# Kernel tuning notes

Hardware: AMD Instinct MI355X
Metric: run time of the kernel (lower is better)

## Reference

```python
import jax, jax.numpy as jnp
import numpy as np

B, S, F, H = 256, 1024, 64, 64

def setup_inputs() -> dict:
    key = jax.random.key(0)
    ks = jax.random.split(key, 6)
    x = jax.random.normal(ks[0], (B, S, F), dtype=jnp.float32)
    # Keras LSTM params: kernel [F,4H], recurrent_kernel [H,4H], bias [4H] (gate order i,f,c,o)
    kernel = jax.random.normal(ks[1], (F, 4 * H), dtype=jnp.float32) * (1.0 / np.sqrt(F))
    rec_kernel = jax.random.normal(ks[2], (H, 4 * H), dtype=jnp.float32) * (1.0 / np.sqrt(H))
    bias = jnp.zeros((4 * H,), dtype=jnp.float32)
    dense_w = jax.random.normal(ks[3], (H, 1), dtype=jnp.float32) * (1.0 / np.sqrt(H))
    dense_b = jnp.zeros((1,), dtype=jnp.float32)
    return {"x": x, "kernel": kernel, "rec_kernel": rec_kernel, "bias": bias,
            "dense_w": dense_w, "dense_b": dense_b}

def reference(x, kernel, rec_kernel, bias, dense_w, dense_b):
    # Precompute input contribution for all timesteps: [B,S,4H]
    xz = jnp.einsum('bsf,fg->bsg', x, kernel) + bias
    xz_t = jnp.transpose(xz, (1, 0, 2))  # [S,B,4H]

    def step(carry, xz_step):
        h, c = carry
        z = xz_step + h @ rec_kernel  # [B,4H]
        zi, zf, zc, zo = jnp.split(z, 4, axis=-1)
        i = jax.nn.sigmoid(zi)
        f = jax.nn.sigmoid(zf)
        o = jax.nn.sigmoid(zo)
        c_new = f * c + i * jnp.tanh(zc)
        h_new = o * jnp.tanh(c_new)
        return (h_new, c_new), h_new

    h0 = jnp.zeros((x.shape[0], rec_kernel.shape[0]), dtype=x.dtype)
    c0 = jnp.zeros_like(h0)
    _, hs = jax.lax.scan(step, (h0, c0), xz_t)  # hs: [S,B,H]
    hs = jnp.transpose(hs, (1, 0, 2))  # [B,S,H]
    out = jax.nn.sigmoid(hs @ dense_w + dense_b)  # [B,S,1]
    return out
```

## Files before the change

kernel.cpp:

```cpp
#include <hip/hip_runtime.h>

typedef __attribute__((ext_vector_type(8))) short short8;
typedef __attribute__((ext_vector_type(4))) float f32x4;

#define SS 1024
#define NBLK 64
#define HROW 72

__device__ __forceinline__ float sigmoidf_(float x) {
    return __builtin_amdgcn_rcpf(1.0f + __expf(-x));
}
__device__ __forceinline__ float tanhf_(float x) {
    return 1.0f - 2.0f * __builtin_amdgcn_rcpf(__expf(2.0f * x) + 1.0f);
}
__device__ __forceinline__ unsigned short f2bf(float f) {
    unsigned int u = __float_as_uint(f);
    u += 0x7fffu + ((u >> 16) & 1u);
    return (unsigned short)(u >> 16);
}
__device__ __forceinline__ float bf2f(unsigned short u) {
    return __uint_as_float((unsigned int)u << 16);
}
__device__ __forceinline__ float h2f_lo(unsigned int u) {
    _Float16 h; unsigned short s = (unsigned short)(u & 0xffffu);
    __builtin_memcpy(&h, &s, 2); return (float)h;
}
__device__ __forceinline__ float h2f_hi(unsigned int u) {
    _Float16 h; unsigned short s = (unsigned short)(u >> 16);
    __builtin_memcpy(&h, &s, 2); return (float)h;
}
__device__ __forceinline__ unsigned int pkf16(float a, float b) {
    auto p = __builtin_amdgcn_cvt_pkrtz(a, b);
    unsigned int u; __builtin_memcpy(&u, &p, 4); return u;
}

#define RAW_BARRIER() asm volatile("s_waitcnt lgkmcnt(0)\n\ts_barrier" ::: "memory")

#define MF(A, Bv, C) __builtin_amdgcn_mfma_f32_16x16x32_bf16(A, Bv, C, 0, 0, 0)

__global__ __launch_bounds__(256)
void xzgemm(const float* __restrict__ x, const float* __restrict__ wk,
            const float* __restrict__ bias, uint2* __restrict__ xzp) {
    const int tid = threadIdx.x;
    const int l   = tid & 63;
    const int w   = tid >> 6;
    const int m   = l & 15;
    const int q   = l >> 4;

    short8 Bf[16][2];
    float  bv[16];
#pragma unroll
    for (int ct = 0; ct < 16; ++ct) {
        bv[ct] = bias[ct * 16 + m];
#pragma unroll
        for (int h2 = 0; h2 < 2; ++h2) {
            short8 v;
#pragma unroll
            for (int j = 0; j < 8; ++j)
                v[j] = (short)f2bf(wk[(h2 * 32 + q * 8 + j) * 256 + ct * 16 + m]);
            Bf[ct][h2] = v;
        }
    }

    const int wt = blockIdx.x * 4 + w;
    for (int it = 0; it < 16; ++it) {
        const int ti = wt * 16 + it;
        const float* __restrict__ xr = x + (size_t)(ti * 16 + m) * 64;
        const float4 a0 = *(const float4*)(xr + q * 8);
        const float4 a1 = *(const float4*)(xr + q * 8 + 4);
        const float4 b0 = *(const float4*)(xr + 32 + q * 8);
        const float4 b1 = *(const float4*)(xr + 32 + q * 8 + 4);
        short8 xa0, xa1;
        xa0[0] = (short)f2bf(a0.x); xa0[1] = (short)f2bf(a0.y);
        xa0[2] = (short)f2bf(a0.z); xa0[3] = (short)f2bf(a0.w);
        xa0[4] = (short)f2bf(a1.x); xa0[5] = (short)f2bf(a1.y);
        xa0[6] = (short)f2bf(a1.z); xa0[7] = (short)f2bf(a1.w);
        xa1[0] = (short)f2bf(b0.x); xa1[1] = (short)f2bf(b0.y);
        xa1[2] = (short)f2bf(b0.z); xa1[3] = (short)f2bf(b0.w);
        xa1[4] = (short)f2bf(b1.x); xa1[5] = (short)f2bf(b1.y);
        xa1[6] = (short)f2bf(b1.z); xa1[7] = (short)f2bf(b1.w);

#pragma unroll
        for (int ctn = 0; ctn < 4; ++ctn) {
            const f32x4 ci = {bv[ctn],      bv[ctn],      bv[ctn],      bv[ctn]};
            const f32x4 cf = {bv[ctn + 4],  bv[ctn + 4],  bv[ctn + 4],  bv[ctn + 4]};
            const f32x4 cc = {bv[ctn + 8],  bv[ctn + 8],  bv[ctn + 8],  bv[ctn + 8]};
            const f32x4 co = {bv[ctn + 12], bv[ctn + 12], bv[ctn + 12], bv[ctn + 12]};
            const f32x4 zi = MF(xa1, Bf[ctn][1],      MF(xa0, Bf[ctn][0],      ci));
            const f32x4 zf = MF(xa1, Bf[ctn + 4][1],  MF(xa0, Bf[ctn + 4][0],  cf));
            const f32x4 zc = MF(xa1, Bf[ctn + 8][1],  MF(xa0, Bf[ctn + 8][0],  cc));
            const f32x4 zo = MF(xa1, Bf[ctn + 12][1], MF(xa0, Bf[ctn + 12][0], co));
            uint2* __restrict__ ob =
                xzp + ((size_t)(ti * 16 + q * 4) * 64 + ctn * 16 + m);
#pragma unroll
            for (int r = 0; r < 4; ++r) {
                uint2 v;
                v.x = pkf16(zi[r], zf[r]);
                v.y = pkf16(zc[r], zo[r]);
                ob[(size_t)r * 64] = v;
            }
        }
    }
}

#define LOADB(VAR, G, KC) do {                                                \
    const int kb = ((KC) << 5) + (q << 3);                                    \
    const int nn = ((G) << 6) + n0;                                           \
    short8 v;                                                                 \
    v[0] = (short)f2bf(rk[(kb + 0) * 256 + nn]);                              \
    v[1] = (short)f2bf(rk[(kb + 1) * 256 + nn]);                              \
    v[2] = (short)f2bf(rk[(kb + 2) * 256 + nn]);                              \
    v[3] = (short)f2bf(rk[(kb + 3) * 256 + nn]);                              \
    v[4] = (short)f2bf(rk[(kb + 4) * 256 + nn]);                              \
    v[5] = (short)f2bf(rk[(kb + 5) * 256 + nn]);                              \
    v[6] = (short)f2bf(rk[(kb + 6) * 256 + nn]);                              \
    v[7] = (short)f2bf(rk[(kb + 7) * 256 + nn]);                              \
    VAR = v; } while (0)

#define REGION(T, PAR, P, DO_O) do {                                           \
    const short8 ha0 = *(const short8*)&hbuf[(PAR) ^ 1][m * HROW + (q << 3)];  \
    const short8 ha1 = *(const short8*)&hbuf[(PAR) ^ 1][m * HROW + 32 + (q << 3)]; \
    const uint2 cur = P;                                                       \
    P = xb[(size_t)(((T) + 2 < SS) ? (T) + 2 : SS - 1) << 6];                  \
    const float vi = h2f_lo(cur.x), vf = h2f_hi(cur.x);                        \
    const float vc = h2f_lo(cur.y), vo = h2f_hi(cur.y);                        \
    const f32x4 cgi = {vi, vi, vi, vi};                                        \
    const f32x4 cgf = {vf, vf, vf, vf};                                        \
    const f32x4 cgc = {vc, vc, vc, vc};                                        \
    const f32x4 cgo = {vo, vo, vo, vo};                                        \
    const f32x4 zc = MF(ha1, BHC1, MF(ha0, BHC0, cgc));                        \
    const f32x4 zo = MF(ha1, BHO1, MF(ha0, BHO0, cgo));                        \
    const f32x4 zi = MF(ha1, BHI1, MF(ha0, BHI0, cgi));                        \
    const f32x4 zf = MF(ha1, BHF1, MF(ha0, BHF0, cgf));                        \
    if (DM == 1 && (DO_O) && w == 0) {                                         \
        const f32x4 zz = {0.f, 0.f, 0.f, 0.f};                                 \
        const f32x4 z4 = MF(ha1, BD1, MF(ha0, BD0, zz));                       \
        if (m == 0) {                                                          \
            out[((size_t)((bb << 2) + q) << 10) + (T) - 1] =                   \
                sigmoidf_(z4[0] + db0);                                        \
        }                                                                      \
    }                                                                          \
    const float tc = tanhf_(zc[0]);                                            \
    const float go = sigmoidf_(zo[0]);                                         \
    const float gi = sigmoidf_(zi[0]);                                         \
    const float gf = sigmoidf_(zf[0]);                                         \
    cc0 = gf * cc0 + gi * tc;                                                  \
    const float h0 = go * tanhf_(cc0);                                         \
    const unsigned short hb16 = f2bf(h0);                                      \
    hbuf[PAR][(q << 2) * HROW + n0] = (short)hb16;                             \
    if (DM == 0) hb[(size_t)(T) << 6] = hb16;                                  \
    RAW_BARRIER();                                                             \
} while (0)

template<int DM>
__global__ __launch_bounds__(256, 1)
void lstm_xz(const uint2* __restrict__ xzu, const float* __restrict__ rk,
             unsigned short* __restrict__ hg, const float* __restrict__ dw,
             const float* __restrict__ db, float* __restrict__ out) {
    const int bb  = blockIdx.x;
    const int tid = threadIdx.x;
    const int l   = tid & 63;
    const int w   = tid >> 6;
    const int m   = l & 15;
    const int q   = l >> 4;
    const int n0  = (w << 4) + m;

    __shared__ short hbuf[2][16 * HROW];

    for (int i = tid; i < 2 * 16 * HROW; i += 256) ((short*)hbuf)[i] = 0;
    __syncthreads();

    short8 BHI0, BHI1, BHF0, BHF1, BHC0, BHC1, BHO0, BHO1;
    LOADB(BHI0, 0, 0); LOADB(BHI1, 0, 1);
    LOADB(BHF0, 1, 0); LOADB(BHF1, 1, 1);
    LOADB(BHC0, 2, 0); LOADB(BHC1, 2, 1);
    LOADB(BHO0, 3, 0); LOADB(BHO1, 3, 1);

    short8 BD0, BD1;
    {
        short8 v0 = {0, 0, 0, 0, 0, 0, 0, 0}, v1 = v0;
        if (m == 0) {
#pragma unroll
            for (int i = 0; i < 8; ++i) v0[i] = (short)f2bf(dw[(q << 3) + i]);
#pragma unroll
            for (int i = 0; i < 8; ++i) v1[i] = (short)f2bf(dw[32 + (q << 3) + i]);
        }
        BD0 = v0; BD1 = v1;
    }
    const float db0 = db[0];

    const size_t base = ((size_t)((bb << 2) + q) << 16) + n0;
    const uint2* __restrict__ xb = xzu + base;
    unsigned short* __restrict__ hb = hg + base;

    uint2 PA = xb[0], PB = xb[64];
    float cc0 = 0.f;

    REGION(0, 0, PA, 0);
    REGION(1, 1, PB, 1);
    for (int t = 2; t < SS; t += 2) {
        REGION(t,     0, PA, 1);
        REGION(t + 1, 1, PB, 1);
    }
    if (DM == 1 && w == 0) {
        const short8 ha0 = *(const short8*)&hbuf[1][m * HROW + (q << 3)];
        const short8 ha1 = *(const short8*)&hbuf[1][m * HROW + 32 + (q << 3)];
        const f32x4 zz = {0.f, 0.f, 0.f, 0.f};
        const f32x4 z4 = MF(ha1, BD1, MF(ha0, BD0, zz));
        if (m == 0) {
            out[((size_t)((bb << 2) + q) << 10) + SS - 1] =
                sigmoidf_(z4[0] + db0);
        }
    }
}

__global__ __launch_bounds__(256)
void dense_out(const unsigned short* __restrict__ hg,
               const float* __restrict__ dw, const float* __restrict__ db,
               float* __restrict__ out) {
    const int row = blockIdx.x * 256 + threadIdx.x;
    const short8* __restrict__ hr = (const short8*)(hg + (size_t)row * 64);
    float acc = db[0];
#pragma unroll
    for (int jj = 0; jj < 8; ++jj) {
        const short8 v = hr[jj];
#pragma unroll
        for (int k = 0; k < 8; ++k)
            acc += bf2f((unsigned short)v[k]) * dw[jj * 8 + k];
    }
    out[row] = sigmoidf_(acc);
}

extern "C" void kernel_launch(void* const* d_in, const int* in_sizes, int n_in,
                              void* d_out, int out_size, void* d_ws, size_t ws_size,
                              hipStream_t stream) {
    const float* x    = (const float*)d_in[0];
    const float* wk   = (const float*)d_in[1];
    const float* rk   = (const float*)d_in[2];
    const float* bias = (const float*)d_in[3];
    const float* dw   = (const float*)d_in[4];
    const float* db   = (const float*)d_in[5];
    float* out = (float*)d_out;

    const size_t XZ_BYTES = (size_t)262144 * 256 * 2;
    const size_t HG_BYTES = (size_t)262144 * 64 * 2;

    uint2* xz = (uint2*)d_ws;
    hipLaunchKernelGGL(xzgemm, dim3(256), dim3(256), 0, stream,
                       x, wk, bias, xz);

    if (ws_size >= XZ_BYTES + HG_BYTES) {
        unsigned short* hg = (unsigned short*)((char*)d_ws + XZ_BYTES);
        hipLaunchKernelGGL((lstm_xz<0>), dim3(NBLK), dim3(256), 0, stream,
                           xz, rk, hg, dw, db, out);
        hipLaunchKernelGGL(dense_out, dim3(1024), dim3(256), 0, stream,
                           hg, dw, db, out);
    } else {
        hipLaunchKernelGGL((lstm_xz<1>), dim3(NBLK), dim3(256), 0, stream,
                           xz, rk, (unsigned short*)nullptr, dw, db, out);
    }
}
```

Baseline: 426.7 us.

## Interleave two independent batch groups per LSTM block, halving block count

```diff
diff --git a/kernel.cpp b/kernel.cpp
--- a/kernel.cpp
+++ b/kernel.cpp
@@ -4,7 +4,7 @@
 typedef __attribute__((ext_vector_type(4))) float f32x4;
 
 #define SS 1024
-#define NBLK 64
+#define NBLK 32
 #define HROW 72
 
 __device__ __forceinline__ float sigmoidf_(float x) {
@@ -63,8 +63,8 @@
     }
 
     const int wt = blockIdx.x * 4 + w;
-    for (int it = 0; it < 16; ++it) {
-        const int ti = wt * 16 + it;
+    for (int it = 0; it < 4; ++it) {
+        const int ti = wt * 4 + it;
         const float* __restrict__ xr = x + (size_t)(ti * 16 + m) * 64;
         const float4 a0 = *(const float4*)(xr + q * 8);
         const float4 a1 = *(const float4*)(xr + q * 8 + 4);
@@ -117,46 +117,55 @@
     v[7] = (short)f2bf(rk[(kb + 7) * 256 + nn]);                              \
     VAR = v; } while (0)
 
-#define REGION(T, PAR, P, DO_O) do {                                           \
-    const short8 ha0 = *(const short8*)&hbuf[(PAR) ^ 1][m * HROW + (q << 3)];  \
-    const short8 ha1 = *(const short8*)&hbuf[(PAR) ^ 1][m * HROW + 32 + (q << 3)]; \
-    const uint2 cur = P;                                                       \
-    P = xb[(size_t)(((T) + 2 < SS) ? (T) + 2 : SS - 1) << 6];                  \
-    const float vi = h2f_lo(cur.x), vf = h2f_hi(cur.x);                        \
-    const float vc = h2f_lo(cur.y), vo = h2f_hi(cur.y);                        \
-    const f32x4 cgi = {vi, vi, vi, vi};                                        \
-    const f32x4 cgf = {vf, vf, vf, vf};                                        \
-    const f32x4 cgc = {vc, vc, vc, vc};                                        \
-    const f32x4 cgo = {vo, vo, vo, vo};                                        \
-    const f32x4 zc = MF(ha1, BHC1, MF(ha0, BHC0, cgc));                        \
-    const f32x4 zo = MF(ha1, BHO1, MF(ha0, BHO0, cgo));                        \
-    const f32x4 zi = MF(ha1, BHI1, MF(ha0, BHI0, cgi));                        \
-    const f32x4 zf = MF(ha1, BHF1, MF(ha0, BHF0, cgf));                        \
-    if (DM == 1 && (DO_O) && w == 0) {                                         \
-        const f32x4 zz = {0.f, 0.f, 0.f, 0.f};                                 \
-        const f32x4 z4 = MF(ha1, BD1, MF(ha0, BD0, zz));                       \
-        if (m == 0) {                                                          \
-            out[((size_t)((bb << 2) + q) << 10) + (T) - 1] =                   \
-                sigmoidf_(z4[0] + db0);                                        \
-        }                                                                      \
-    }                                                                          \
-    const float tc = tanhf_(zc[0]);                                            \
-    const float go = sigmoidf_(zo[0]);                                         \
-    const float gi = sigmoidf_(zi[0]);                                         \
-    const float gf = sigmoidf_(zf[0]);                                         \
-    cc0 = gf * cc0 + gi * tc;                                                  \
-    const float h0 = go * tanhf_(cc0);                                         \
-    const unsigned short hb16 = f2bf(h0);                                      \
-    hbuf[PAR][(q << 2) * HROW + n0] = (short)hb16;                             \
-    if (DM == 0) hb[(size_t)(T) << 6] = hb16;                                  \
+#define REGION2(T, PAR, Pa, Pb) do {                                           \
+    const short8 a0 = *(const short8*)&hbufA[(PAR) ^ 1][m * HROW + (q << 3)];  \
+    const short8 a1 = *(const short8*)&hbufA[(PAR) ^ 1][m * HROW + 32 + (q << 3)]; \
+    const short8 b0 = *(const short8*)&hbufB[(PAR) ^ 1][m * HROW + (q << 3)];  \
+    const short8 b1 = *(const short8*)&hbufB[(PAR) ^ 1][m * HROW + 32 + (q << 3)]; \
+    const uint2 curA = Pa; const uint2 curB = Pb;                              \
+    { const size_t xo = (size_t)(((T) + 2 < SS) ? (T) + 2 : SS - 1) << 6;      \
+      Pa = xbA[xo]; Pb = xbB[xo]; }                                            \
+    const float viA = h2f_lo(curA.x), vfA = h2f_hi(curA.x);                    \
+    const float vcA = h2f_lo(curA.y), voA = h2f_hi(curA.y);                    \
+    const float viB = h2f_lo(curB.x), vfB = h2f_hi(curB.x);                    \
+    const float vcB = h2f_lo(curB.y), voB = h2f_hi(curB.y);                    \
+    const f32x4 cgcA = {vcA, vcA, vcA, vcA};                                   \
+    const f32x4 cgoA = {voA, voA, voA, voA};                                   \
+    const f32x4 cgiA = {viA, viA, viA, viA};                                   \
+    const f32x4 cgfA = {vfA, vfA, vfA, vfA};                                   \
+    const f32x4 cgcB = {vcB, vcB, vcB, vcB};                                   \
+    const f32x4 cgoB = {voB, voB, voB, voB};                                   \
+    const f32x4 cgiB = {viB, viB, viB, viB};                                   \
+    const f32x4 cgfB = {vfB, vfB, vfB, vfB};                                   \
+    const f32x4 zcA = MF(a1, BHC1, MF(a0, BHC0, cgcA));                        \
+    const f32x4 zcB = MF(b1, BHC1, MF(b0, BHC0, cgcB));                        \
+    const f32x4 zoA = MF(a1, BHO1, MF(a0, BHO0, cgoA));                        \
+    const f32x4 zoB = MF(b1, BHO1, MF(b0, BHO0, cgoB));                        \
+    const f32x4 ziA = MF(a1, BHI1, MF(a0, BHI0, cgiA));                        \
+    const f32x4 ziB = MF(b1, BHI1, MF(b0, BHI0, cgiB));                        \
+    const f32x4 zfA = MF(a1, BHF1, MF(a0, BHF0, cgfA));                        \
+    const f32x4 zfB = MF(b1, BHF1, MF(b0, BHF0, cgfB));                        \
+    const float tcA = tanhf_(zcA[0]);                                          \
+    const float tcB = tanhf_(zcB[0]);                                          \
+    const float goA = sigmoidf_(zoA[0]), giA = sigmoidf_(ziA[0]);              \
+    const float gfA = sigmoidf_(zfA[0]);                                       \
+    const float goB = sigmoidf_(zoB[0]), giB = sigmoidf_(ziB[0]);              \
+    const float gfB = sigmoidf_(zfB[0]);                                       \
+    ccA = gfA * ccA + giA * tcA;                                               \
+    ccB = gfB * ccB + giB * tcB;                                               \
+    const float hA = goA * tanhf_(ccA);                                        \
+    const float hB = goB * tanhf_(ccB);                                        \
+    const unsigned short hA16 = f2bf(hA), hB16 = f2bf(hB);                     \
+    hbufA[PAR][(q << 2) * HROW + n0] = (short)hA16;                            \
+    hbufB[PAR][(q << 2) * HROW + n0] = (short)hB16;                            \
+    hbA[(size_t)(T) << 6] = hA16;                                              \
+    hbB[(size_t)(T) << 6] = hB16;                                              \
     RAW_BARRIER();                                                             \
 } while (0)
 
-template<int DM>
 __global__ __launch_bounds__(256, 1)
-void lstm_xz(const uint2* __restrict__ xzu, const float* __restrict__ rk,
-             unsigned short* __restrict__ hg, const float* __restrict__ dw,
-             const float* __restrict__ db, float* __restrict__ out) {
+void lstm_g2(const uint2* __restrict__ xzu, const float* __restrict__ rk,
+             unsigned short* __restrict__ hg) {
     const int bb  = blockIdx.x;
     const int tid = threadIdx.x;
     const int l   = tid & 63;
@@ -165,9 +174,13 @@
     const int q   = l >> 4;
     const int n0  = (w << 4) + m;
 
-    __shared__ short hbuf[2][16 * HROW];
-
-    for (int i = tid; i < 2 * 16 * HROW; i += 256) ((short*)hbuf)[i] = 0;
+    __shared__ short hbufA[2][16 * HROW];
+    __shared__ short hbufB[2][16 * HROW];
+
+    for (int i = tid; i < 2 * 16 * HROW; i += 256) {
+        ((short*)hbufA)[i] = 0;
+        ((short*)hbufB)[i] = 0;
+    }
     __syncthreads();
 
     short8 BHI0, BHI1, BHF0, BHF1, BHC0, BHC1, BHO0, BHO1;
@@ -176,41 +189,22 @@
     LOADB(BHC0, 2, 0); LOADB(BHC1, 2, 1);
     LOADB(BHO0, 3, 0); LOADB(BHO1, 3, 1);
 
-    short8 BD0, BD1;
-    {
-        short8 v0 = {0, 0, 0, 0, 0, 0, 0, 0}, v1 = v0;
-        if (m == 0) {
-#pragma unroll
-            for (int i = 0; i < 8; ++i) v0[i] = (short)f2bf(dw[(q << 3) + i]);
-#pragma unroll
-            for (int i = 0; i < 8; ++i) v1[i] = (short)f2bf(dw[32 + (q << 3) + i]);
-        }
-        BD0 = v0; BD1 = v1;
-    }
-    const float db0 = db[0];
-
-    const size_t base = ((size_t)((bb << 2) + q) << 16) + n0;
-    const uint2* __restrict__ xb = xzu + base;
-    unsigned short* __restrict__ hb = hg + base;
-
-    uint2 PA = xb[0], PB = xb[64];
-    float cc0 = 0.f;
-
-    REGION(0, 0, PA, 0);
-    REGION(1, 1, PB, 1);
+    const size_t baseA = ((size_t)((bb << 3) + q) << 16) + n0;
+    const size_t baseB = ((size_t)((bb << 3) + 4 + q) << 16) + n0;
+    const uint2* __restrict__ xbA = xzu + baseA;
+    const uint2* __restrict__ xbB = xzu + baseB;
+    unsigned short* __restrict__ hbA = hg + baseA;
+    unsigned short* __restrict__ hbB = hg + baseB;
+
+    uint2 QA = xbA[0], RA = xbA[64];
+    uint2 QB = xbB[0], RB = xbB[64];
+    float ccA = 0.f, ccB = 0.f;
+
+    REGION2(0, 0, QA, QB);
+    REGION2(1, 1, RA, RB);
     for (int t = 2; t < SS; t += 2) {
-        REGION(t,     0, PA, 1);
-        REGION(t + 1, 1, PB, 1);
-    }
-    if (DM == 1 && w == 0) {
-        const short8 ha0 = *(const short8*)&hbuf[1][m * HROW + (q << 3)];
-        const short8 ha1 = *(const short8*)&hbuf[1][m * HROW + 32 + (q << 3)];
-        const f32x4 zz = {0.f, 0.f, 0.f, 0.f};
-        const f32x4 z4 = MF(ha1, BD1, MF(ha0, BD0, zz));
-        if (m == 0) {
-            out[((size_t)((bb << 2) + q) << 10) + SS - 1] =
-                sigmoidf_(z4[0] + db0);
-        }
+        REGION2(t,     0, QA, QB);
+        REGION2(t + 1, 1, RA, RB);
     }
 }
 
@@ -243,20 +237,13 @@
     float* out = (float*)d_out;
 
     const size_t XZ_BYTES = (size_t)262144 * 256 * 2;
-    const size_t HG_BYTES = (size_t)262144 * 64 * 2;
-
     uint2* xz = (uint2*)d_ws;
-    hipLaunchKernelGGL(xzgemm, dim3(256), dim3(256), 0, stream,
+    unsigned short* hg = (unsigned short*)((char*)d_ws + XZ_BYTES);
+
+    hipLaunchKernelGGL(xzgemm, dim3(1024), dim3(256), 0, stream,
                        x, wk, bias, xz);
-
-    if (ws_size >= XZ_BYTES + HG_BYTES) {
-        unsigned short* hg = (unsigned short*)((char*)d_ws + XZ_BYTES);
-        hipLaunchKernelGGL((lstm_xz<0>), dim3(NBLK), dim3(256), 0, stream,
-                           xz, rk, hg, dw, db, out);
-        hipLaunchKernelGGL(dense_out, dim3(1024), dim3(256), 0, stream,
-                           hg, dw, db, out);
-    } else {
-        hipLaunchKernelGGL((lstm_xz<1>), dim3(NBLK), dim3(256), 0, stream,
-                           xz, rk, (unsigned short*)nullptr, dw, db, out);
-    }
-}
+    hipLaunchKernelGGL(lstm_g2, dim3(NBLK), dim3(256), 0, stream,
+                       xz, rk, hg);
+    hipLaunchKernelGGL(dense_out, dim3(1024), dim3(256), 0, stream,
+                       hg, dw, db, out);
+}
```

New measurement: 607.8 us. 42.4% more time.

## Fuse input projection into recurrent kernel via producer warps and LDS ring

Applied to the files above, without the earlier changes.

```diff
diff --git a/kernel.cpp b/kernel.cpp
--- a/kernel.cpp
+++ b/kernel.cpp
@@ -38,108 +38,34 @@
 
 #define MF(A, Bv, C) __builtin_amdgcn_mfma_f32_16x16x32_bf16(A, Bv, C, 0, 0, 0)
 
-__global__ __launch_bounds__(256)
-void xzgemm(const float* __restrict__ x, const float* __restrict__ wk,
-            const float* __restrict__ bias, uint2* __restrict__ xzp) {
-    const int tid = threadIdx.x;
-    const int l   = tid & 63;
-    const int w   = tid >> 6;
-    const int m   = l & 15;
-    const int q   = l >> 4;
-
-    short8 Bf[16][2];
-    float  bv[16];
-#pragma unroll
-    for (int ct = 0; ct < 16; ++ct) {
-        bv[ct] = bias[ct * 16 + m];
-#pragma unroll
-        for (int h2 = 0; h2 < 2; ++h2) {
-            short8 v;
-#pragma unroll
-            for (int j = 0; j < 8; ++j)
-                v[j] = (short)f2bf(wk[(h2 * 32 + q * 8 + j) * 256 + ct * 16 + m]);
-            Bf[ct][h2] = v;
-        }
-    }
-
-    const int wt = blockIdx.x * 4 + w;
-    for (int it = 0; it < 16; ++it) {
-        const int ti = wt * 16 + it;
-        const float* __restrict__ xr = x + (size_t)(ti * 16 + m) * 64;
-        const float4 a0 = *(const float4*)(xr + q * 8);
-        const float4 a1 = *(const float4*)(xr + q * 8 + 4);
-        const float4 b0 = *(const float4*)(xr + 32 + q * 8);
-        const float4 b1 = *(const float4*)(xr + 32 + q * 8 + 4);
-        short8 xa0, xa1;
-        xa0[0] = (short)f2bf(a0.x); xa0[1] = (short)f2bf(a0.y);
-        xa0[2] = (short)f2bf(a0.z); xa0[3] = (short)f2bf(a0.w);
-        xa0[4] = (short)f2bf(a1.x); xa0[5] = (short)f2bf(a1.y);
-        xa0[6] = (short)f2bf(a1.z); xa0[7] = (short)f2bf(a1.w);
-        xa1[0] = (short)f2bf(b0.x); xa1[1] = (short)f2bf(b0.y);
-        xa1[2] = (short)f2bf(b0.z); xa1[3] = (short)f2bf(b0.w);
-        xa1[4] = (short)f2bf(b1.x); xa1[5] = (short)f2bf(b1.y);
-        xa1[6] = (short)f2bf(b1.z); xa1[7] = (short)f2bf(b1.w);
-
-#pragma unroll
-        for (int ctn = 0; ctn < 4; ++ctn) {
-            const f32x4 ci = {bv[ctn],      bv[ctn],      bv[ctn],      bv[ctn]};
-            const f32x4 cf = {bv[ctn + 4],  bv[ctn + 4],  bv[ctn + 4],  bv[ctn + 4]};
-            const f32x4 cc = {bv[ctn + 8],  bv[ctn + 8],  bv[ctn + 8],  bv[ctn + 8]};
-            const f32x4 co = {bv[ctn + 12], bv[ctn + 12], bv[ctn + 12], bv[ctn + 12]};
-            const f32x4 zi = MF(xa1, Bf[ctn][1],      MF(xa0, Bf[ctn][0],      ci));
-            const f32x4 zf = MF(xa1, Bf[ctn + 4][1],  MF(xa0, Bf[ctn + 4][0],  cf));
-            const f32x4 zc = MF(xa1, Bf[ctn + 8][1],  MF(xa0, Bf[ctn + 8][0],  cc));
-            const f32x4 zo = MF(xa1, Bf[ctn + 12][1], MF(xa0, Bf[ctn + 12][0], co));
-            uint2* __restrict__ ob =
-                xzp + ((size_t)(ti * 16 + q * 4) * 64 + ctn * 16 + m);
-#pragma unroll
-            for (int r = 0; r < 4; ++r) {
-                uint2 v;
-                v.x = pkf16(zi[r], zf[r]);
-                v.y = pkf16(zc[r], zo[r]);
-                ob[(size_t)r * 64] = v;
-            }
-        }
-    }
-}
-
-#define LOADB(VAR, G, KC) do {                                                \
+
+#define LOADB(VAR, G, KC, SRC, NN) do {                                       \
     const int kb = ((KC) << 5) + (q << 3);                                    \
-    const int nn = ((G) << 6) + n0;                                           \
     short8 v;                                                                 \
-    v[0] = (short)f2bf(rk[(kb + 0) * 256 + nn]);                              \
-    v[1] = (short)f2bf(rk[(kb + 1) * 256 + nn]);                              \
-    v[2] = (short)f2bf(rk[(kb + 2) * 256 + nn]);                              \
-    v[3] = (short)f2bf(rk[(kb + 3) * 256 + nn]);                              \
-    v[4] = (short)f2bf(rk[(kb + 4) * 256 + nn]);                              \
-    v[5] = (short)f2bf(rk[(kb + 5) * 256 + nn]);                              \
-    v[6] = (short)f2bf(rk[(kb + 6) * 256 + nn]);                              \
-    v[7] = (short)f2bf(rk[(kb + 7) * 256 + nn]);                              \
+    v[0] = (short)f2bf(SRC[(kb + 0) * 256 + (NN)]);                           \
+    v[1] = (short)f2bf(SRC[(kb + 1) * 256 + (NN)]);                           \
+    v[2] = (short)f2bf(SRC[(kb + 2) * 256 + (NN)]);                           \
+    v[3] = (short)f2bf(SRC[(kb + 3) * 256 + (NN)]);                           \
+    v[4] = (short)f2bf(SRC[(kb + 4) * 256 + (NN)]);                           \
+    v[5] = (short)f2bf(SRC[(kb + 5) * 256 + (NN)]);                           \
+    v[6] = (short)f2bf(SRC[(kb + 6) * 256 + (NN)]);                           \
+    v[7] = (short)f2bf(SRC[(kb + 7) * 256 + (NN)]);                           \
     VAR = v; } while (0)
 
-#define REGION(T, PAR, P, DO_O) do {                                           \
+#define CREGION(T, PAR) do {                                                   \
     const short8 ha0 = *(const short8*)&hbuf[(PAR) ^ 1][m * HROW + (q << 3)];  \
     const short8 ha1 = *(const short8*)&hbuf[(PAR) ^ 1][m * HROW + 32 + (q << 3)]; \
-    const uint2 cur = P;                                                       \
-    P = xb[(size_t)(((T) + 2 < SS) ? (T) + 2 : SS - 1) << 6];                  \
+    const uint2 cur = ring[(T) & 1][q][n0];                                    \
     const float vi = h2f_lo(cur.x), vf = h2f_hi(cur.x);                        \
     const float vc = h2f_lo(cur.y), vo = h2f_hi(cur.y);                        \
+    const f32x4 cgc = {vc, vc, vc, vc};                                        \
+    const f32x4 cgo = {vo, vo, vo, vo};                                        \
     const f32x4 cgi = {vi, vi, vi, vi};                                        \
     const f32x4 cgf = {vf, vf, vf, vf};                                        \
-    const f32x4 cgc = {vc, vc, vc, vc};                                        \
-    const f32x4 cgo = {vo, vo, vo, vo};                                        \
     const f32x4 zc = MF(ha1, BHC1, MF(ha0, BHC0, cgc));                        \
     const f32x4 zo = MF(ha1, BHO1, MF(ha0, BHO0, cgo));                        \
     const f32x4 zi = MF(ha1, BHI1, MF(ha0, BHI0, cgi));                        \
     const f32x4 zf = MF(ha1, BHF1, MF(ha0, BHF0, cgf));                        \
-    if (DM == 1 && (DO_O) && w == 0) {                                         \
-        const f32x4 zz = {0.f, 0.f, 0.f, 0.f};                                 \
-        const f32x4 z4 = MF(ha1, BD1, MF(ha0, BD0, zz));                       \
-        if (m == 0) {                                                          \
-            out[((size_t)((bb << 2) + q) << 10) + (T) - 1] =                   \
-                sigmoidf_(z4[0] + db0);                                        \
-        }                                                                      \
-    }                                                                          \
     const float tc = tanhf_(zc[0]);                                            \
     const float go = sigmoidf_(zo[0]);                                         \
     const float gi = sigmoidf_(zi[0]);                                         \
@@ -148,68 +74,106 @@
     const float h0 = go * tanhf_(cc0);                                         \
     const unsigned short hb16 = f2bf(h0);                                      \
     hbuf[PAR][(q << 2) * HROW + n0] = (short)hb16;                             \
-    if (DM == 0) hb[(size_t)(T) << 6] = hb16;                                  \
+    hb[(size_t)(T) << 6] = hb16;                                               \
     RAW_BARRIER();                                                             \
 } while (0)
 
-template<int DM>
-__global__ __launch_bounds__(256, 1)
-void lstm_xz(const uint2* __restrict__ xzu, const float* __restrict__ rk,
-             unsigned short* __restrict__ hg, const float* __restrict__ dw,
-             const float* __restrict__ db, float* __restrict__ out) {
+#define PPROD(S, RPS, F0, F1, F2, F3) do {                                     \
+    if ((S) < SS) {                                                            \
+        short8 xa0, xa1;                                                       \
+        xa0[0] = (short)f2bf(F0.x); xa0[1] = (short)f2bf(F0.y);                \
+        xa0[2] = (short)f2bf(F0.z); xa0[3] = (short)f2bf(F0.w);                \
+        xa0[4] = (short)f2bf(F1.x); xa0[5] = (short)f2bf(F1.y);                \
+        xa0[6] = (short)f2bf(F1.z); xa0[7] = (short)f2bf(F1.w);                \
+        xa1[0] = (short)f2bf(F2.x); xa1[1] = (short)f2bf(F2.y);                \
+        xa1[2] = (short)f2bf(F2.z); xa1[3] = (short)f2bf(F2.w);                \
+        xa1[4] = (short)f2bf(F3.x); xa1[5] = (short)f2bf(F3.y);                \
+        xa1[6] = (short)f2bf(F3.z); xa1[7] = (short)f2bf(F3.w);                \
+        const f32x4 zi = MF(xa1, WI1, MF(xa0, WI0, cbi));                      \
+        const f32x4 zf = MF(xa1, WF1, MF(xa0, WF0, cbf));                      \
+        const f32x4 zc = MF(xa1, WC1, MF(xa0, WC0, cbc));                      \
+        const f32x4 zo = MF(xa1, WO1, MF(xa0, WO0, cbo));                      \
+        uint2 v;                                                               \
+        v.x = pkf16(zi[0], zf[0]);                                             \
+        v.y = pkf16(zc[0], zo[0]);                                             \
+        ring[RPS][q][pw16m] = v;                                               \
+    }                                                                          \
+    { const int sn = ((S) + 2 < SS) ? (S) + 2 : SS - 1;                        \
+      const float* __restrict__ xs = xp + ((size_t)sn << 6);                   \
+      F0 = *(const float4*)(xs + (q << 3));                                    \
+      F1 = *(const float4*)(xs + (q << 3) + 4);                                \
+      F2 = *(const float4*)(xs + 32 + (q << 3));                               \
+      F3 = *(const float4*)(xs + 36 + (q << 3)); }                             \
+    RAW_BARRIER();                                                             \
+} while (0)
+
+__global__ __launch_bounds__(512, 1)
+void lstm_fused(const float* __restrict__ x, const float* __restrict__ wk,
+                const float* __restrict__ rk, const float* __restrict__ bias,
+                unsigned short* __restrict__ hg) {
     const int bb  = blockIdx.x;
     const int tid = threadIdx.x;
     const int l   = tid & 63;
     const int w   = tid >> 6;
     const int m   = l & 15;
     const int q   = l >> 4;
-    const int n0  = (w << 4) + m;
 
     __shared__ short hbuf[2][16 * HROW];
-
-    for (int i = tid; i < 2 * 16 * HROW; i += 256) ((short*)hbuf)[i] = 0;
+    __shared__ uint2 ring[2][4][64];
+
+    for (int i = tid; i < 2 * 16 * HROW; i += 512) ((short*)hbuf)[i] = 0;
     __syncthreads();
 
-    short8 BHI0, BHI1, BHF0, BHF1, BHC0, BHC1, BHO0, BHO1;
-    LOADB(BHI0, 0, 0); LOADB(BHI1, 0, 1);
-    LOADB(BHF0, 1, 0); LOADB(BHF1, 1, 1);
-    LOADB(BHC0, 2, 0); LOADB(BHC1, 2, 1);
-    LOADB(BHO0, 3, 0); LOADB(BHO1, 3, 1);
-
-    short8 BD0, BD1;
-    {
-        short8 v0 = {0, 0, 0, 0, 0, 0, 0, 0}, v1 = v0;
-        if (m == 0) {
-#pragma unroll
-            for (int i = 0; i < 8; ++i) v0[i] = (short)f2bf(dw[(q << 3) + i]);
-#pragma unroll
-            for (int i = 0; i < 8; ++i) v1[i] = (short)f2bf(dw[32 + (q << 3) + i]);
+    if (w < 4) {
+        const int n0 = (w << 4) + m;
+        short8 BHI0, BHI1, BHF0, BHF1, BHC0, BHC1, BHO0, BHO1;
+        LOADB(BHI0, 0, 0, rk, (0 << 6) + n0); LOADB(BHI1, 0, 1, rk, (0 << 6) + n0);
+        LOADB(BHF0, 1, 0, rk, (1 << 6) + n0); LOADB(BHF1, 1, 1, rk, (1 << 6) + n0);
+        LOADB(BHC0, 2, 0, rk, (2 << 6) + n0); LOADB(BHC1, 2, 1, rk, (2 << 6) + n0);
+        LOADB(BHO0, 3, 0, rk, (3 << 6) + n0); LOADB(BHO1, 3, 1, rk, (3 << 6) + n0);
+
+        unsigned short* __restrict__ hb =
+            hg + ((size_t)((bb << 2) + q) << 16) + n0;
+        float cc0 = 0.f;
+
+        RAW_BARRIER();
+        for (int t = 0; t < SS; t += 2) {
+            CREGION(t,     0);
+            CREGION(t + 1, 1);
         }
-        BD0 = v0; BD1 = v1;
-    }
-    const float db0 = db[0];
-
-    const size_t base = ((size_t)((bb << 2) + q) << 16) + n0;
-    const uint2* __restrict__ xb = xzu + base;
-    unsigned short* __restrict__ hb = hg + base;
-
-    uint2 PA = xb[0], PB = xb[64];
-    float cc0 = 0.f;
-
-    REGION(0, 0, PA, 0);
-    REGION(1, 1, PB, 1);
-    for (int t = 2; t < SS; t += 2) {
-        REGION(t,     0, PA, 1);
-        REGION(t + 1, 1, PB, 1);
-    }
-    if (DM == 1 && w == 0) {
-        const short8 ha0 = *(const short8*)&hbuf[1][m * HROW + (q << 3)];
-        const short8 ha1 = *(const short8*)&hbuf[1][m * HROW + 32 + (q << 3)];
-        const f32x4 zz = {0.f, 0.f, 0.f, 0.f};
-        const f32x4 z4 = MF(ha1, BD1, MF(ha0, BD0, zz));
-        if (m == 0) {
-            out[((size_t)((bb << 2) + q) << 10) + SS - 1] =
-                sigmoidf_(z4[0] + db0);
+    } else {
+        const int pw16m = ((w - 4) << 4) + m;
+        short8 WI0, WI1, WF0, WF1, WC0, WC1, WO0, WO1;
+        LOADB(WI0, 0, 0, wk, (0 << 6) + pw16m); LOADB(WI1, 0, 1, wk, (0 << 6) + pw16m);
+        LOADB(WF0, 1, 0, wk, (1 << 6) + pw16m); LOADB(WF1, 1, 1, wk, (1 << 6) + pw16m);
+        LOADB(WC0, 2, 0, wk, (2 << 6) + pw16m); LOADB(WC1, 2, 1, wk, (2 << 6) + pw16m);
+        LOADB(WO0, 3, 0, wk, (3 << 6) + pw16m); LOADB(WO1, 3, 1, wk, (3 << 6) + pw16m);
+
+        const float bi = bias[(0 << 6) + pw16m];
+        const float bf = bias[(1 << 6) + pw16m];
+        const float bc = bias[(2 << 6) + pw16m];
+        const float bo = bias[(3 << 6) + pw16m];
+        const f32x4 cbi = {bi, bi, bi, bi};
+        const f32x4 cbf = {bf, bf, bf, bf};
+        const f32x4 cbc = {bc, bc, bc, bc};
+        const f32x4 cbo = {bo, bo, bo, bo};
+
+        const float* __restrict__ xp =
+            x + ((size_t)((bb << 2) + (m >> 2)) << 16);
+
+        float4 XA0 = *(const float4*)(xp + (q << 3));
+        float4 XA1 = *(const float4*)(xp + (q << 3) + 4);
+        float4 XA2 = *(const float4*)(xp + 32 + (q << 3));
+        float4 XA3 = *(const float4*)(xp + 36 + (q << 3));
+        float4 XB0 = *(const float4*)(xp + 64 + (q << 3));
+        float4 XB1 = *(const float4*)(xp + 64 + (q << 3) + 4);
+        float4 XB2 = *(const float4*)(xp + 96 + (q << 3));
+        float4 XB3 = *(const float4*)(xp + 100 + (q << 3));
+
+        PPROD(0, 0, XA0, XA1, XA2, XA3);
+        for (int t = 0; t < SS; t += 2) {
+            PPROD(t + 1, 1, XB0, XB1, XB2, XB3);
+            PPROD(t + 2, 0, XA0, XA1, XA2, XA3);
         }
     }
 }
@@ -242,21 +206,10 @@
     const float* db   = (const float*)d_in[5];
     float* out = (float*)d_out;
 
-    const size_t XZ_BYTES = (size_t)262144 * 256 * 2;
-    const size_t HG_BYTES = (size_t)262144 * 64 * 2;
-
-    uint2* xz = (uint2*)d_ws;
-    hipLaunchKernelGGL(xzgemm, dim3(256), dim3(256), 0, stream,
-                       x, wk, bias, xz);
-
-    if (ws_size >= XZ_BYTES + HG_BYTES) {
-        unsigned short* hg = (unsigned short*)((char*)d_ws + XZ_BYTES);
-        hipLaunchKernelGGL((lstm_xz<0>), dim3(NBLK), dim3(256), 0, stream,
-                           xz, rk, hg, dw, db, out);
-        hipLaunchKernelGGL(dense_out, dim3(1024), dim3(256), 0, stream,
-                           hg, dw, db, out);
-    } else {
-        hipLaunchKernelGGL((lstm_xz<1>), dim3(NBLK), dim3(256), 0, stream,
-                           xz, rk, (unsigned short*)nullptr, dw, db, out);
-    }
-}
+    unsigned short* hg = (unsigned short*)d_ws;
+
+    hipLaunchKernelGGL(lstm_fused, dim3(NBLK), dim3(512), 0, stream,
+                       x, wk, rk, bias, hg);
+    hipLaunchKernelGGL(dense_out, dim3(1024), dim3(256), 0, stream,
+                       hg, dw, db, out);
+}
```

New measurement: 457.3 us. 7.2% more time.
